# Kernel tuning notes

Hardware: AMD Instinct MI355X
Metric: run time of the kernel (lower is better)

## Reference

```python
import jax, jax.numpy as jnp
import numpy as np

BINS = 10
N, C = 32768, 1000


def setup_inputs() -> dict:
    key = jax.random.key(0)
    k1, k2 = jax.random.split(key)
    x = jax.random.normal(k1, (N, C), dtype=jnp.float32)
    target = jax.random.randint(k2, (N,), 0, C, dtype=jnp.int64)
    return {"x": x, "target": target}


def reference(x, target):
    n_rows, n_cls = x.shape
    onehot = jax.nn.one_hot(target, n_cls, dtype=x.dtype)  # [N, C]
    # gradient density, detached as in the original (g = |sigmoid(x).detach() - onehot|)
    g = jnp.abs(jax.lax.stop_gradient(jax.nn.sigmoid(x)) - onehot)
    # bin index: edges are i/BINS with last edge nudged to 1+1e-6, so g==1 lands in last bin.
    bin_idx = jnp.minimum((g * BINS).astype(jnp.int32), BINS - 1)  # [N, C]
    # single-pass histogram over all N*C elements
    counts = jnp.zeros((BINS,), dtype=x.dtype).at[bin_idx.reshape(-1)].add(1.0)
    n_nonempty = jnp.sum(counts > 0).astype(x.dtype)  # >=1 since every element falls in a bin
    # per-element weight = tot / num_in_bin (tot = 1), then /= n and /= tot
    safe_counts = jnp.maximum(counts, 1.0)
    w = (1.0 / safe_counts)[bin_idx] / n_nonempty  # [N, C]
    # weights = 1 / (w / row_target_weight) = w_target / w ; clamp > 1 to 1
    w_target = jnp.take_along_axis(w, target[:, None].astype(jnp.int32), axis=1)  # [N, 1]
    weights = jnp.minimum(w_target / w, 1.0)
    weighted_x = x + jnp.log(weights)
    logp = jax.nn.log_softmax(weighted_x, axis=1)
    loss = -jnp.sum(onehot * logp) / n_rows
    return loss
```

## Files before the change

### kernel.cpp

```cpp
#include <hip/hip_runtime.h>

#define N_ROWS   32768
#define N_COLS   1000
#define NBINS    10
#define K1_BLKS  2048
#define K2_BLKS  128
#define C0_TOTAL 32768000.0f

__device__ __forceinline__ int bin_of(float v) {
    int b = 0;
    b += (v >= -2.19722458f);
    b += (v >= -1.38629436f);
    b += (v >= -0.84729786f);
    b += (v >= -0.40546511f);
    b += (v >=  0.0f);
    b += (v >=  0.40546511f);
    b += (v >=  0.84729786f);
    b += (v >=  1.38629436f);
    b += (v >=  2.19722458f);
    return b;
}

#define BFLY_F(v) do { v += __shfl_xor(v, 32); v += __shfl_xor(v, 16); \
                       v += __shfl_xor(v, 8);  v += __shfl_xor(v, 4);  \
                       v += __shfl_xor(v, 2);  v += __shfl_xor(v, 1); } while (0)
#define BFLY_U(v) do { v += (unsigned)__shfl_xor((int)(v), 32); \
                       v += (unsigned)__shfl_xor((int)(v), 16); \
                       v += (unsigned)__shfl_xor((int)(v), 8);  \
                       v += (unsigned)__shfl_xor((int)(v), 4);  \
                       v += (unsigned)__shfl_xor((int)(v), 2);  \
                       v += (unsigned)__shfl_xor((int)(v), 1); } while (0)

extern "C" __global__ __launch_bounds__(256)
void ghm_pass1(const float* __restrict__ x, const int* __restrict__ target,
               unsigned int* __restrict__ partialC, float* __restrict__ Trows,
               unsigned int* __restrict__ ticket) {
    __shared__ unsigned int cw[4][9];
    const int tid = threadIdx.x, wid = tid >> 6, lane = tid & 63;
    const int bid = blockIdx.x;
    if (bid == 0 && tid == 0) *ticket = 0u;

    const float E1 = -2.19722458f, E2 = -1.38629436f, E3 = -0.84729786f,
                E4 = -0.40546511f, E5 = 0.0f,         E6 = 0.40546511f,
                E7 = 0.84729786f,  E8 = 1.38629436f,  E9 = 2.19722458f;

    unsigned int C1=0,C2=0,C3=0,C4=0,C5=0,C6=0,C7=0,C8=0,C9=0;

#pragma unroll 1
    for (int r = 0; r < 4; ++r) {
        const int row = bid * 4 + wid + r * (K1_BLKS * 4);
        const int t = target[row];
        const float* xrow = x + (size_t)row * N_COLS;
        const float xt = xrow[t];
        float T0=0,T1=0,T2=0,T3=0,T4=0,T5=0,T6=0,T7=0,T8=0,T9=0;
#pragma unroll
        for (int k = 0; k < 4; ++k) {
            const int f4 = k * 64 + lane;
            if (f4 < 250) {
                const float4 v = reinterpret_cast<const float4*>(xrow)[f4];
#define ACC(c) do { const float e_ = __expf(c); T0 += e_; \
                T1 += ((c) >= E1) ? e_ : 0.f;  C1 += ((c) >= E1); \
                T2 += ((c) >= E2) ? e_ : 0.f;  C2 += ((c) >= E2); \
                T3 += ((c) >= E3) ? e_ : 0.f;  C3 += ((c) >= E3); \
                T4 += ((c) >= E4) ? e_ : 0.f;  C4 += ((c) >= E4); \
                T5 += ((c) >= E5) ? e_ : 0.f;  C5 += ((c) >= E5); \
                T6 += ((c) >= E6) ? e_ : 0.f;  C6 += ((c) >= E6); \
                T7 += ((c) >= E7) ? e_ : 0.f;  C7 += ((c) >= E7); \
                T8 += ((c) >= E8) ? e_ : 0.f;  C8 += ((c) >= E8); \
                T9 += ((c) >= E9) ? e_ : 0.f;  C9 += ((c) >= E9); } while (0)
                ACC(v.x); ACC(v.y); ACC(v.z); ACC(v.w);
#undef ACC
            }
        }
        if (lane == 0) {
            const float nxt = -xt;
            C1 += (unsigned)(nxt >= E1) - (unsigned)(xt >= E1);
            C2 += (unsigned)(nxt >= E2) - (unsigned)(xt >= E2);
            C3 += (unsigned)(nxt >= E3) - (unsigned)(xt >= E3);
            C4 += (unsigned)(nxt >= E4) - (unsigned)(xt >= E4);
            C5 += (unsigned)(nxt >= E5) - (unsigned)(xt >= E5);
            C6 += (unsigned)(nxt >= E6) - (unsigned)(xt >= E6);
            C7 += (unsigned)(nxt >= E7) - (unsigned)(xt >= E7);
            C8 += (unsigned)(nxt >= E8) - (unsigned)(xt >= E8);
            C9 += (unsigned)(nxt >= E9) - (unsigned)(xt >= E9);
        }
        BFLY_F(T0); BFLY_F(T1); BFLY_F(T2); BFLY_F(T3); BFLY_F(T4);
        BFLY_F(T5); BFLY_F(T6); BFLY_F(T7); BFLY_F(T8); BFLY_F(T9);
        if (lane == 0) {
            float4* dst = reinterpret_cast<float4*>(Trows + (size_t)row * 12);
            dst[0] = make_float4(T0, T1, T2, T3);
            dst[1] = make_float4(T4, T5, T6, T7);
            dst[2] = make_float4(T8, T9, xt, 0.f);
        }
    }

    BFLY_U(C1); BFLY_U(C2); BFLY_U(C3); BFLY_U(C4); BFLY_U(C5);
    BFLY_U(C6); BFLY_U(C7); BFLY_U(C8); BFLY_U(C9);
    if (lane == 0) {
        cw[wid][0]=C1; cw[wid][1]=C2; cw[wid][2]=C3; cw[wid][3]=C4;
        cw[wid][4]=C5; cw[wid][5]=C6; cw[wid][6]=C7; cw[wid][7]=C8; cw[wid][8]=C9;
    }
    __syncthreads();
    if (tid < 9)
        partialC[tid * K1_BLKS + bid] = cw[0][tid] + cw[1][tid] + cw[2][tid] + cw[3][tid];
}

extern "C" __global__ __launch_bounds__(256)
void ghm_pass2(const unsigned int* __restrict__ partialC, const float* __restrict__ Trows,
               float* __restrict__ blockloss, unsigned int* __restrict__ ticket,
               float* __restrict__ out) {
    __shared__ float Cl[11];
    __shared__ float cnt[NBINS];
    __shared__ float Wt[NBINS][NBINS];
    __shared__ float red[4];
    __shared__ int   lastFlag;
    const int tid = threadIdx.x, wid = tid >> 6, lane = tid & 63;
    const int bid = blockIdx.x;

    for (int b = wid; b < 9; b += 4) {
        unsigned int s = 0;
        for (int k = lane; k < K1_BLKS; k += 64) s += partialC[b * K1_BLKS + k];
        BFLY_U(s);
        if (lane == 0) Cl[b + 1] = (float)s;
    }
    if (tid == 0) { Cl[0] = C0_TOTAL; Cl[10] = 0.0f; }
    __syncthreads();
    if (tid < NBINS) cnt[tid] = Cl[tid] - Cl[tid + 1];
    __syncthreads();
    if (tid < NBINS * NBINS) {
        const int tau = tid / NBINS, b = tid % NBINS;
        Wt[tau][b] = fminf(cnt[b] / cnt[tau], 1.0f);
    }
    __syncthreads();

    const int row = bid * 256 + tid;
    const float4* Tp = reinterpret_cast<const float4*>(Trows + (size_t)row * 12);
    const float4 t0 = Tp[0];
    const float4 t1 = Tp[1];
    const float4 t2 = Tp[2];
    const float xt  = t2.z;
    const int   bt  = bin_of(-xt);
    const int   bxt = bin_of(xt);
    const float* W  = Wt[bt];
    float d = W[0] * t0.x;
    d += (W[1] - W[0]) * t0.y;
    d += (W[2] - W[1]) * t0.z;
    d += (W[3] - W[2]) * t0.w;
    d += (W[4] - W[3]) * t1.x;
    d += (W[5] - W[4]) * t1.y;
    d += (W[6] - W[5]) * t1.z;
    d += (W[7] - W[6]) * t1.w;
    d += (W[8] - W[7]) * t2.x;
    d += (W[9] - W[8]) * t2.y;
    d += __expf(xt) * (1.0f - W[bxt]);
    float loss = __logf(d) - xt;

    BFLY_F(loss);
    if (lane == 0) red[wid] = loss;
    __syncthreads();
    if (tid == 0) {
        blockloss[bid] = (red[0] + red[1]) + (red[2] + red[3]);
        __threadfence();
        lastFlag = (atomicAdd(ticket, 1u) == K2_BLKS - 1);
    }
    __syncthreads();
    if (lastFlag) {
        __threadfence();
        float s = 0.0f;
        if (tid < K2_BLKS)
            s = __hip_atomic_load(&blockloss[tid], __ATOMIC_RELAXED, __HIP_MEMORY_SCOPE_AGENT);
        BFLY_F(s);
        if (lane == 0) red[wid] = s;
        __syncthreads();
        if (tid == 0)
            out[0] = ((red[0] + red[1]) + (red[2] + red[3])) / (float)N_ROWS;
    }
}

extern "C" void kernel_launch(void* const* d_in, const int* in_sizes, int n_in,
                              void* d_out, int out_size, void* d_ws, size_t ws_size,
                              hipStream_t stream) {
    const float* x      = (const float*)d_in[0];
    const int*   target = (const int*)d_in[1];
    unsigned int* partialC  = (unsigned int*)d_ws;
    unsigned int* ticket    = (unsigned int*)((char*)d_ws + 81920);
    float*        blockloss = (float*)((char*)d_ws + 82048);
    float*        Trows     = (float*)((char*)d_ws + 98304);

    hipLaunchKernelGGL(ghm_pass1, dim3(K1_BLKS), dim3(256), 0, stream,
                       x, target, partialC, Trows, ticket);
    hipLaunchKernelGGL(ghm_pass2, dim3(K2_BLKS), dim3(256), 0, stream,
                       partialC, Trows, blockloss, ticket, (float*)d_out);
}
```

Baseline: 59.24 us.

## Fuse histogram and loss passes into one kernel with ticket-gated tail blocks

Merges the two kernels into one launch. The last 128 blocks to take a ticket spin-wait until every block has published its partial bin counts, then run the former second pass. This is meant to remove the second launch and the gap between kernels. It also changes the row mapping so that 16 lanes handle each row and each block covers 16 rows, with a 16-lane butterfly reduction. In exchange it adds a memset of the tickets before the launch, a spin-wait that depends on all blocks making forward progress, and a different load pattern per row.

```diff
diff --git a/kernel.cpp b/kernel.cpp
--- a/kernel.cpp
+++ b/kernel.cpp
@@ -3,8 +3,8 @@
 #define N_ROWS   32768
 #define N_COLS   1000
 #define NBINS    10
-#define K1_BLKS  2048
-#define K2_BLKS  128
+#define BLKS     2048
+#define K2BLKS   128
 #define C0_TOTAL 32768000.0f
 
 __device__ __forceinline__ int bin_of(float v) {
@@ -21,77 +21,87 @@
     return b;
 }
 
-#define BFLY_F(v) do { v += __shfl_xor(v, 32); v += __shfl_xor(v, 16); \
-                       v += __shfl_xor(v, 8);  v += __shfl_xor(v, 4);  \
-                       v += __shfl_xor(v, 2);  v += __shfl_xor(v, 1); } while (0)
-#define BFLY_U(v) do { v += (unsigned)__shfl_xor((int)(v), 32); \
-                       v += (unsigned)__shfl_xor((int)(v), 16); \
-                       v += (unsigned)__shfl_xor((int)(v), 8);  \
-                       v += (unsigned)__shfl_xor((int)(v), 4);  \
-                       v += (unsigned)__shfl_xor((int)(v), 2);  \
-                       v += (unsigned)__shfl_xor((int)(v), 1); } while (0)
+#define BFLY_F(v)  do { v += __shfl_xor(v, 32); v += __shfl_xor(v, 16); \
+                        v += __shfl_xor(v, 8);  v += __shfl_xor(v, 4);  \
+                        v += __shfl_xor(v, 2);  v += __shfl_xor(v, 1); } while (0)
+#define BFLY16_F(v) do { v += __shfl_xor(v, 8); v += __shfl_xor(v, 4);  \
+                         v += __shfl_xor(v, 2); v += __shfl_xor(v, 1); } while (0)
+#define BFLY_U(v)  do { v += (unsigned)__shfl_xor((int)(v), 32); \
+                        v += (unsigned)__shfl_xor((int)(v), 16); \
+                        v += (unsigned)__shfl_xor((int)(v), 8);  \
+                        v += (unsigned)__shfl_xor((int)(v), 4);  \
+                        v += (unsigned)__shfl_xor((int)(v), 2);  \
+                        v += (unsigned)__shfl_xor((int)(v), 1); } while (0)
 
 extern "C" __global__ __launch_bounds__(256)
-void ghm_pass1(const float* __restrict__ x, const int* __restrict__ target,
+void ghm_fused(const float* __restrict__ x, const int* __restrict__ target,
+               unsigned int* __restrict__ ticket1, unsigned int* __restrict__ ticket2,
                unsigned int* __restrict__ partialC, float* __restrict__ Trows,
-               unsigned int* __restrict__ ticket) {
+               float* __restrict__ blockloss, float* __restrict__ out) {
     __shared__ unsigned int cw[4][9];
+    __shared__ int s_old;
     const int tid = threadIdx.x, wid = tid >> 6, lane = tid & 63;
+    const int sub = lane & 15;
     const int bid = blockIdx.x;
-    if (bid == 0 && tid == 0) *ticket = 0u;
+
+    const int row = bid * 16 + (tid >> 4);
+    const float* xrow = x + (size_t)row * N_COLS;
+
+    int   t  = 0;
+    float xt = 0.0f;
+    if (sub == 0) t = target[row];
 
     const float E1 = -2.19722458f, E2 = -1.38629436f, E3 = -0.84729786f,
                 E4 = -0.40546511f, E5 = 0.0f,         E6 = 0.40546511f,
                 E7 = 0.84729786f,  E8 = 1.38629436f,  E9 = 2.19722458f;
 
     unsigned int C1=0,C2=0,C3=0,C4=0,C5=0,C6=0,C7=0,C8=0,C9=0;
-
-#pragma unroll 1
-    for (int r = 0; r < 4; ++r) {
-        const int row = bid * 4 + wid + r * (K1_BLKS * 4);
-        const int t = target[row];
-        const float* xrow = x + (size_t)row * N_COLS;
-        const float xt = xrow[t];
-        float T0=0,T1=0,T2=0,T3=0,T4=0,T5=0,T6=0,T7=0,T8=0,T9=0;
-#pragma unroll
-        for (int k = 0; k < 4; ++k) {
-            const int f4 = k * 64 + lane;
-            if (f4 < 250) {
-                const float4 v = reinterpret_cast<const float4*>(xrow)[f4];
+    float T0=0,T1=0,T2=0,T3=0,T4=0,T5=0,T6=0,T7=0,T8=0,T9=0;
+
+    if (sub == 0) xt = xrow[t];
+
 #define ACC(c) do { const float e_ = __expf(c); T0 += e_; \
-                T1 += ((c) >= E1) ? e_ : 0.f;  C1 += ((c) >= E1); \
-                T2 += ((c) >= E2) ? e_ : 0.f;  C2 += ((c) >= E2); \
-                T3 += ((c) >= E3) ? e_ : 0.f;  C3 += ((c) >= E3); \
-                T4 += ((c) >= E4) ? e_ : 0.f;  C4 += ((c) >= E4); \
-                T5 += ((c) >= E5) ? e_ : 0.f;  C5 += ((c) >= E5); \
-                T6 += ((c) >= E6) ? e_ : 0.f;  C6 += ((c) >= E6); \
-                T7 += ((c) >= E7) ? e_ : 0.f;  C7 += ((c) >= E7); \
-                T8 += ((c) >= E8) ? e_ : 0.f;  C8 += ((c) >= E8); \
-                T9 += ((c) >= E9) ? e_ : 0.f;  C9 += ((c) >= E9); } while (0)
-                ACC(v.x); ACC(v.y); ACC(v.z); ACC(v.w);
+        T1 += ((c) >= E1) ? e_ : 0.f;  C1 += ((c) >= E1); \
+        T2 += ((c) >= E2) ? e_ : 0.f;  C2 += ((c) >= E2); \
+        T3 += ((c) >= E3) ? e_ : 0.f;  C3 += ((c) >= E3); \
+        T4 += ((c) >= E4) ? e_ : 0.f;  C4 += ((c) >= E4); \
+        T5 += ((c) >= E5) ? e_ : 0.f;  C5 += ((c) >= E5); \
+        T6 += ((c) >= E6) ? e_ : 0.f;  C6 += ((c) >= E6); \
+        T7 += ((c) >= E7) ? e_ : 0.f;  C7 += ((c) >= E7); \
+        T8 += ((c) >= E8) ? e_ : 0.f;  C8 += ((c) >= E8); \
+        T9 += ((c) >= E9) ? e_ : 0.f;  C9 += ((c) >= E9); } while (0)
+
+#pragma unroll 5
+    for (int k = 0; k < 15; ++k) {
+        const float4 v = reinterpret_cast<const float4*>(xrow)[k * 16 + sub];
+        ACC(v.x); ACC(v.y); ACC(v.z); ACC(v.w);
+    }
+    if (sub < 10) {
+        const float4 v = reinterpret_cast<const float4*>(xrow)[240 + sub];
+        ACC(v.x); ACC(v.y); ACC(v.z); ACC(v.w);
+    }
 #undef ACC
-            }
-        }
-        if (lane == 0) {
-            const float nxt = -xt;
-            C1 += (unsigned)(nxt >= E1) - (unsigned)(xt >= E1);
-            C2 += (unsigned)(nxt >= E2) - (unsigned)(xt >= E2);
-            C3 += (unsigned)(nxt >= E3) - (unsigned)(xt >= E3);
-            C4 += (unsigned)(nxt >= E4) - (unsigned)(xt >= E4);
-            C5 += (unsigned)(nxt >= E5) - (unsigned)(xt >= E5);
-            C6 += (unsigned)(nxt >= E6) - (unsigned)(xt >= E6);
-            C7 += (unsigned)(nxt >= E7) - (unsigned)(xt >= E7);
-            C8 += (unsigned)(nxt >= E8) - (unsigned)(xt >= E8);
-            C9 += (unsigned)(nxt >= E9) - (unsigned)(xt >= E9);
-        }
-        BFLY_F(T0); BFLY_F(T1); BFLY_F(T2); BFLY_F(T3); BFLY_F(T4);
-        BFLY_F(T5); BFLY_F(T6); BFLY_F(T7); BFLY_F(T8); BFLY_F(T9);
-        if (lane == 0) {
-            float4* dst = reinterpret_cast<float4*>(Trows + (size_t)row * 12);
-            dst[0] = make_float4(T0, T1, T2, T3);
-            dst[1] = make_float4(T4, T5, T6, T7);
-            dst[2] = make_float4(T8, T9, xt, 0.f);
-        }
+
+    if (sub == 0) {
+        const float nxt = -xt;
+        C1 += (unsigned)(nxt >= E1) - (unsigned)(xt >= E1);
+        C2 += (unsigned)(nxt >= E2) - (unsigned)(xt >= E2);
+        C3 += (unsigned)(nxt >= E3) - (unsigned)(xt >= E3);
+        C4 += (unsigned)(nxt >= E4) - (unsigned)(xt >= E4);
+        C5 += (unsigned)(nxt >= E5) - (unsigned)(xt >= E5);
+        C6 += (unsigned)(nxt >= E6) - (unsigned)(xt >= E6);
+        C7 += (unsigned)(nxt >= E7) - (unsigned)(xt >= E7);
+        C8 += (unsigned)(nxt >= E8) - (unsigned)(xt >= E8);
+        C9 += (unsigned)(nxt >= E9) - (unsigned)(xt >= E9);
+    }
+
+    BFLY16_F(T0); BFLY16_F(T1); BFLY16_F(T2); BFLY16_F(T3); BFLY16_F(T4);
+    BFLY16_F(T5); BFLY16_F(T6); BFLY16_F(T7); BFLY16_F(T8); BFLY16_F(T9);
+    if (sub == 0) {
+        float4* dst = reinterpret_cast<float4*>(Trows + (size_t)row * 12);
+        dst[0] = make_float4(T0, T1, T2, T3);
+        dst[1] = make_float4(T4, T5, T6, T7);
+        dst[2] = make_float4(T8, T9, xt, 0.f);
     }
 
     BFLY_U(C1); BFLY_U(C2); BFLY_U(C3); BFLY_U(C4); BFLY_U(C5);
@@ -102,24 +112,36 @@
     }
     __syncthreads();
     if (tid < 9)
-        partialC[tid * K1_BLKS + bid] = cw[0][tid] + cw[1][tid] + cw[2][tid] + cw[3][tid];
-}
-
-extern "C" __global__ __launch_bounds__(256)
-void ghm_pass2(const unsigned int* __restrict__ partialC, const float* __restrict__ Trows,
-               float* __restrict__ blockloss, unsigned int* __restrict__ ticket,
-               float* __restrict__ out) {
+        partialC[tid * BLKS + bid] = cw[0][tid] + cw[1][tid] + cw[2][tid] + cw[3][tid];
+
+    if (tid == 0) {
+        __threadfence();
+        s_old = (int)atomicAdd(ticket1, 1u);
+    }
+    __syncthreads();
+    const int old = s_old;
+    if (old < BLKS - K2BLKS) return;
+
+    if (tid == 0) {
+        long guard = 0;
+        while (__hip_atomic_load(ticket1, __ATOMIC_ACQUIRE, __HIP_MEMORY_SCOPE_AGENT)
+               < (unsigned)BLKS) {
+            __builtin_amdgcn_s_sleep(16);
+            if (++guard > 100000000L) break;
+        }
+    }
+    __syncthreads();
+
     __shared__ float Cl[11];
     __shared__ float cnt[NBINS];
     __shared__ float Wt[NBINS][NBINS];
     __shared__ float red[4];
     __shared__ int   lastFlag;
-    const int tid = threadIdx.x, wid = tid >> 6, lane = tid & 63;
-    const int bid = blockIdx.x;
+    const int bid2 = old - (BLKS - K2BLKS);
 
     for (int b = wid; b < 9; b += 4) {
         unsigned int s = 0;
-        for (int k = lane; k < K1_BLKS; k += 64) s += partialC[b * K1_BLKS + k];
+        for (int k = lane; k < BLKS; k += 64) s += partialC[b * BLKS + k];
         BFLY_U(s);
         if (lane == 0) Cl[b + 1] = (float)s;
     }
@@ -133,14 +155,14 @@
     }
     __syncthreads();
 
-    const int row = bid * 256 + tid;
-    const float4* Tp = reinterpret_cast<const float4*>(Trows + (size_t)row * 12);
+    const int row2 = bid2 * 256 + tid;
+    const float4* Tp = reinterpret_cast<const float4*>(Trows + (size_t)row2 * 12);
     const float4 t0 = Tp[0];
     const float4 t1 = Tp[1];
     const float4 t2 = Tp[2];
-    const float xt  = t2.z;
-    const int   bt  = bin_of(-xt);
-    const int   bxt = bin_of(xt);
+    const float xt2 = t2.z;
+    const int   bt  = bin_of(-xt2);
+    const int   bxt = bin_of(xt2);
     const float* W  = Wt[bt];
     float d = W[0] * t0.x;
     d += (W[1] - W[0]) * t0.y;
@@ -152,22 +174,22 @@
     d += (W[7] - W[6]) * t1.w;
     d += (W[8] - W[7]) * t2.x;
     d += (W[9] - W[8]) * t2.y;
-    d += __expf(xt) * (1.0f - W[bxt]);
-    float loss = __logf(d) - xt;
+    d += __expf(xt2) * (1.0f - W[bxt]);
+    float loss = __logf(d) - xt2;
 
     BFLY_F(loss);
     if (lane == 0) red[wid] = loss;
     __syncthreads();
     if (tid == 0) {
-        blockloss[bid] = (red[0] + red[1]) + (red[2] + red[3]);
+        blockloss[bid2] = (red[0] + red[1]) + (red[2] + red[3]);
         __threadfence();
-        lastFlag = (atomicAdd(ticket, 1u) == K2_BLKS - 1);
+        lastFlag = (atomicAdd(ticket2, 1u) == K2BLKS - 1);
     }
     __syncthreads();
     if (lastFlag) {
         __threadfence();
         float s = 0.0f;
-        if (tid < K2_BLKS)
+        if (tid < K2BLKS)
             s = __hip_atomic_load(&blockloss[tid], __ATOMIC_RELAXED, __HIP_MEMORY_SCOPE_AGENT);
         BFLY_F(s);
         if (lane == 0) red[wid] = s;
@@ -182,13 +204,14 @@
                               hipStream_t stream) {
     const float* x      = (const float*)d_in[0];
     const int*   target = (const int*)d_in[1];
-    unsigned int* partialC  = (unsigned int*)d_ws;
-    unsigned int* ticket    = (unsigned int*)((char*)d_ws + 81920);
-    float*        blockloss = (float*)((char*)d_ws + 82048);
-    float*        Trows     = (float*)((char*)d_ws + 98304);
-
-    hipLaunchKernelGGL(ghm_pass1, dim3(K1_BLKS), dim3(256), 0, stream,
-                       x, target, partialC, Trows, ticket);
-    hipLaunchKernelGGL(ghm_pass2, dim3(K2_BLKS), dim3(256), 0, stream,
-                       partialC, Trows, blockloss, ticket, (float*)d_out);
+    unsigned int* ticket1   = (unsigned int*)d_ws;
+    unsigned int* ticket2   = (unsigned int*)((char*)d_ws + 4);
+    float*        blockloss = (float*)((char*)d_ws + 64);
+    unsigned int* partialC  = (unsigned int*)((char*)d_ws + 1024);
+    float*        Trows     = (float*)((char*)d_ws + 74752);
+
+    hipMemsetAsync(d_ws, 0, 8, stream);
+    hipLaunchKernelGGL(ghm_fused, dim3(BLKS), dim3(256), 0, stream,
+                       x, target, ticket1, ticket2, partialC, Trows, blockloss,
+                       (float*)d_out);
 }
```

Measured after the change: 125.3 us. 2.12x slower.
